# Kernel optimization log

Hardware: AMD Instinct MI355X
Metric: run time of the kernel (lower is better)

The kernel has to match this reference:

```python
import jax, jax.numpy as jnp
import numpy as np
from jax import lax

N, L = 4000, 128          # total sentences, sentence length
VOCAB = 50002             # 50000 words + unk + blk
VEC_DIM, POS_DIM = 50, 5
EMB = VEC_DIM + 2 * POS_DIM   # 60
HID = 230
NPOS = 201                # 2*max_pos_length+1
NBAG, BAGSZ = 500, 8
NREL = 25


def setup_inputs() -> dict:
    key = jax.random.key(0)
    ks = jax.random.split(key, 10)
    X = jax.random.randint(ks[0], (N, L), 0, 50000)
    pos1 = jax.random.randint(ks[1], (N, L), 0, NPOS)
    pos2 = jax.random.randint(ks[2], (N, L), 0, NPOS)
    mask = jnp.zeros((N, L), dtype=jnp.int64)       # unused by CNN encoder
    length = jnp.full((N,), L, dtype=jnp.int64)     # unused by CNN encoder
    starts = jnp.arange(NBAG) * BAGSZ
    scope = jnp.stack([starts, starts + BAGSZ], axis=1)  # [NBAG, 2] contiguous bags
    relation = jax.random.randint(ks[3], (NBAG,), 0, NREL)
    word_emb = jax.random.normal(ks[4], (VOCAB, VEC_DIM), jnp.float32) * 0.1
    pos1_emb = jax.random.normal(ks[5], (NPOS, POS_DIM), jnp.float32) * 0.1
    pos2_emb = jax.random.normal(ks[6], (NPOS, POS_DIM), jnp.float32) * 0.1
    conv_w = jax.random.normal(ks[7], (HID, EMB, 3), jnp.float32) * (1.0 / np.sqrt(EMB * 3))
    conv_b = jnp.zeros((HID,), jnp.float32)
    rel_w = jax.random.normal(ks[8], (NREL, HID), jnp.float32) * (1.0 / np.sqrt(HID))
    rel_b = jnp.zeros((NREL,), jnp.float32)
    return {"X": X, "pos1": pos1, "pos2": pos2, "mask": mask, "length": length,
            "scope": scope, "relation": relation, "word_emb": word_emb,
            "pos1_emb": pos1_emb, "pos2_emb": pos2_emb, "conv_w": conv_w,
            "conv_b": conv_b, "rel_w": rel_w, "rel_b": rel_b}


def reference(X, pos1, pos2, mask, length, scope, relation,
              word_emb, pos1_emb, pos2_emb, conv_w, conv_b, rel_w, rel_b):
    # --- word_pos_embedding: gather + concat -> [N, L, EMB]
    emb = jnp.concatenate([word_emb[X], pos1_emb[pos1], pos2_emb[pos2]], axis=-1)
    # --- CNN encoder: conv1d(k=3, same pad) -> max-pool over seq -> relu
    h = lax.conv_general_dilated(
        emb.transpose(0, 2, 1), conv_w, window_strides=(1,), padding='SAME',
        dimension_numbers=('NCH', 'OIH', 'NCH'))  # [N, HID, L]
    h = jax.nn.relu(jnp.max(h + conv_b[None, :, None], axis=2))  # [N, HID]
    # (dropout p=0.0 -> identity)
    # --- ragged per-bag softmax attention pooling (training path, relation given)
    sizes = scope[:, 1] - scope[:, 0]
    bag_ids = jnp.repeat(jnp.arange(NBAG), sizes, total_repeat_length=N)  # [N]
    rel_q = rel_w[relation]                       # [NBAG, HID] attention queries
    logits = jnp.sum(h * rel_q[bag_ids], axis=-1)  # [N]
    m = jax.ops.segment_max(logits, bag_ids, num_segments=NBAG)
    e = jnp.exp(logits - m[bag_ids])
    denom = jax.ops.segment_sum(e, bag_ids, num_segments=NBAG)
    alpha = e / denom[bag_ids]                     # per-bag softmax weights
    bag_rep = jax.ops.segment_sum(alpha[:, None] * h, bag_ids, num_segments=NBAG)  # [NBAG, HID]
    # --- relation classifier
    return bag_rep @ rel_w.T + rel_b               # [NBAG, NREL]
```

## Files before the change

### kernel.cpp

```cpp
#include <hip/hip_runtime.h>
#include <hip/hip_bf16.h>

#define NSENT 4000
#define LSEQ  128
#define VEC   50
#define POS   5
#define EMBD  60
#define HIDD  230
#define HSTR  232
#define NBAG  500
#define NREL  25
#define NTILEP 16
#define KSTEPS 6
#define ESTR  72
#define SLOTS 130
#define SSTR  (SLOTS * ESTR)

typedef __attribute__((ext_vector_type(8))) short short8;
typedef __attribute__((ext_vector_type(4))) float f32x4;

__device__ __forceinline__ unsigned short f2bf(float f) {
    union { float f; unsigned u; } v; v.f = f;
    unsigned u = v.u + 0x7FFF + ((v.u >> 16) & 1);
    return (unsigned short)(u >> 16);
}

__device__ __forceinline__ unsigned pk(float a, float b) {
    __hip_bfloat162 h = __float22bfloat162_rn(float2{a, b});
    union { __hip_bfloat162 h; unsigned u; } c; c.h = h;
    return c.u;
}

__global__ __launch_bounds__(256) void prep_b(const float* __restrict__ conv_w,
                                              unsigned short* __restrict__ Bfrag) {
    int idx = blockIdx.x * 256 + threadIdx.x;
    if (idx >= NTILEP * KSTEPS * 64 * 8) return;
    int j    = idx & 7;
    int lane = (idx >> 3) & 63;
    int t    = idx >> 9;
    int ks   = t % KSTEPS;
    int nt   = t / KSTEPS;
    int c    = nt * 16 + (lane & 15);
    int klin = ks * 32 + (lane >> 4) * 8 + j;
    int tap  = klin >> 6;
    int e    = klin & 63;
    float v  = 0.f;
    if (c < HIDD) {
        int eidx = -1;
        if (e < 50)                 eidx = e;
        else if (e >= 52 && e < 56) eidx = 50 + (e - 52);
        else if (e >= 56 && e < 60) eidx = 55 + (e - 56);
        else if (e == 60)           eidx = 54;
        else if (e == 62)           eidx = 59;
        if (eidx >= 0) v = conv_w[(c * EMBD + eidx) * 3 + tap];
    }
    Bfrag[idx] = f2bf(v);
}

__global__ __launch_bounds__(512, 4) void encoder(
    const int*   __restrict__ X,  const int* __restrict__ P1, const int* __restrict__ P2,
    const float* __restrict__ wemb, const float* __restrict__ p1emb, const float* __restrict__ p2emb,
    const unsigned short* __restrict__ Bfrag, const float* __restrict__ conv_b,
    float* __restrict__ H)
{
    __shared__ unsigned short embS[2 * SSTR];
    __shared__ int xS[2 * LSEQ], p1S[2 * LSEQ], p2S[2 * LSEQ];
    const int b2 = blockIdx.x * 2, tid = threadIdx.x;
    const int lane = tid & 63;
    const int wave = __builtin_amdgcn_readfirstlane(tid >> 6);
    const int nt0  = wave * 2;
    const int m    = lane & 15;
    const int quad = lane >> 4;

    short8 Bw[2][KSTEPS];
    #pragma unroll
    for (int t = 0; t < 2; ++t)
        #pragma unroll
        for (int ks = 0; ks < KSTEPS; ++ks)
            Bw[t][ks] = *(const short8*)(Bfrag + ((size_t)((nt0 + t) * KSTEPS + ks) * 64 + lane) * 8);

    #pragma unroll
    for (int it = 0; it < 2; ++it) {
        int i = tid + it * 512;
        if (i < 768) {
            int which = i >> 8, l2 = i & 255;
            const int* src = (which == 0) ? X : (which == 1) ? P1 : P2;
            int v = src[(size_t)b2 * LSEQ + l2];
            int* dst = (which == 0) ? xS : (which == 1) ? p1S : p2S;
            dst[l2] = v;
        } else {
            int t = i - 768;
            if (t < 128) {
                int sent = t >> 6;
                int r = (t & 32) ? (SLOTS - 1) : 0;
                *(unsigned*)(embS + sent * SSTR + r * ESTR + (t & 31) * 2) = 0u;
            }
        }
    }
    __syncthreads();

    #pragma unroll
    for (int it = 0; it < (2 * LSEQ * 16) / 512; ++it) {
        int i = tid + it * 512;
        int sent = i >> 11, rem = i & 2047;
        int l = rem >> 4, j = rem & 15;
        int li = sent * LSEQ + l;
        unsigned short* dst = embS + sent * SSTR + (l + 1) * ESTR;
        uint2 v;
        if (j < 13) {
            const float* src = wemb + (size_t)xS[li] * VEC + j * 4;
            float2 fa = *(const float2*)(src);
            float a2 = 0.f, a3 = 0.f;
            if (j < 12) { float2 fb = *(const float2*)(src + 2); a2 = fb.x; a3 = fb.y; }
            v.x = pk(fa.x, fa.y); v.y = pk(a2, a3);
        } else if (j == 13) {
            const float* p = p1emb + p1S[li] * POS;
            v.x = pk(p[0], p[1]); v.y = pk(p[2], p[3]);
        } else if (j == 14) {
            const float* p = p2emb + p2S[li] * POS;
            v.x = pk(p[0], p[1]); v.y = pk(p[2], p[3]);
        } else {
            float a = p1emb[p1S[li] * POS + 4];
            float b = p2emb[p2S[li] * POS + 4];
            v.x = pk(a, 0.f); v.y = pk(b, 0.f);
        }
        *(uint2*)(dst + (j < 13 ? j * 4 : 52 + (j - 13) * 4)) = v;
    }
    __syncthreads();

    #pragma unroll 1
    for (int s = 0; s < 2; ++s) {
        const unsigned short* eb = embS + s * SSTR;
        float maxv[2][4];
        #pragma unroll
        for (int t = 0; t < 2; ++t)
            #pragma unroll
            for (int r = 0; r < 4; ++r) maxv[t][r] = -1e30f;

        #pragma unroll
        for (int mt = 0; mt < 8; ++mt) {
            short8 A[KSTEPS];
            #pragma unroll
            for (int ks = 0; ks < KSTEPS; ++ks) {
                int tap = ks >> 1;
                int col = (ks & 1) * 32 + quad * 8;
                int row = mt * 16 + m + tap;
                A[ks] = *(const short8*)(eb + row * ESTR + col);
            }
            f32x4 acc[2];
            #pragma unroll
            for (int t = 0; t < 2; ++t) acc[t] = (f32x4){0.f, 0.f, 0.f, 0.f};
            #pragma unroll
            for (int ks = 0; ks < KSTEPS; ++ks)
                #pragma unroll
                for (int t = 0; t < 2; ++t)
                    acc[t] = __builtin_amdgcn_mfma_f32_16x16x32_bf16(A[ks], Bw[t][ks], acc[t], 0, 0, 0);
            #pragma unroll
            for (int t = 0; t < 2; ++t)
                #pragma unroll
                for (int r = 0; r < 4; ++r)
                    maxv[t][r] = fmaxf(maxv[t][r], acc[t][r]);
        }

        #pragma unroll
        for (int t = 0; t < 2; ++t) {
            float v = fmaxf(fmaxf(maxv[t][0], maxv[t][1]),
                            fmaxf(maxv[t][2], maxv[t][3]));
            v = fmaxf(v, __shfl_xor(v, 16));
            v = fmaxf(v, __shfl_xor(v, 32));
            int c = (nt0 + t) * 16 + lane;
            if (lane < 16 && c < HIDD)
                H[(size_t)(b2 + s) * HSTR + c] = fmaxf(v + conv_b[c], 0.f);
        }
    }
}

__global__ __launch_bounds__(64) void attn(
    const float* __restrict__ H, const float* __restrict__ rel_w, const float* __restrict__ rel_b,
    const int* __restrict__ relation, const int* __restrict__ scope,
    float* __restrict__ out)
{
    const int b = blockIdx.x, lane = threadIdx.x;
    const int start = scope[2 * b];
    int ns = scope[2 * b + 1] - start;
    if (ns > 8) ns = 8;
    const int rel = relation[b];

    float q[4], h[8][4];
    #pragma unroll
    for (int k = 0; k < 4; ++k) {
        int c = lane + 64 * k;
        q[k] = (c < HIDD) ? rel_w[rel * HIDD + c] : 0.f;
    }
    #pragma unroll
    for (int s = 0; s < 8; ++s)
        #pragma unroll
        for (int k = 0; k < 4; ++k) {
            int c = lane + 64 * k;
            h[s][k] = (s < ns && c < HIDD) ? H[(size_t)(start + s) * HSTR + c] : 0.f;
        }

    float logit[8];
    #pragma unroll
    for (int s = 0; s < 8; ++s) {
        float t = q[0] * h[s][0] + q[1] * h[s][1] + q[2] * h[s][2] + q[3] * h[s][3];
        #pragma unroll
        for (int off = 32; off > 0; off >>= 1) t += __shfl_xor(t, off);
        logit[s] = t;
    }

    float mx = -1e30f;
    for (int s = 0; s < ns; ++s) mx = fmaxf(mx, logit[s]);
    float a[8], den = 0.f;
    #pragma unroll
    for (int s = 0; s < 8; ++s) { a[s] = (s < ns) ? expf(logit[s] - mx) : 0.f; den += a[s]; }
    float inv = 1.f / den;

    float rep[4];
    #pragma unroll
    for (int k = 0; k < 4; ++k) {
        float r = 0.f;
        #pragma unroll
        for (int s = 0; s < 8; ++s) r += a[s] * h[s][k];
        rep[k] = r * inv;
    }

    #pragma unroll 5
    for (int g = 0; g < NREL; ++g) {
        float t = 0.f;
        #pragma unroll
        for (int k = 0; k < 4; ++k) {
            int c = lane + 64 * k;
            t += (c < HIDD) ? rel_w[g * HIDD + c] * rep[k] : 0.f;
        }
        #pragma unroll
        for (int off = 32; off > 0; off >>= 1) t += __shfl_xor(t, off);
        if (lane == 0) out[b * NREL + g] = t + rel_b[g];
    }
}

extern "C" void kernel_launch(void* const* d_in, const int* in_sizes, int n_in,
                              void* d_out, int out_size, void* d_ws, size_t ws_size,
                              hipStream_t stream) {
    const int*   X        = (const int*)d_in[0];
    const int*   P1       = (const int*)d_in[1];
    const int*   P2       = (const int*)d_in[2];
    const int*   scope    = (const int*)d_in[5];
    const int*   relation = (const int*)d_in[6];
    const float* wemb     = (const float*)d_in[7];
    const float* p1emb    = (const float*)d_in[8];
    const float* p2emb    = (const float*)d_in[9];
    const float* conv_w   = (const float*)d_in[10];
    const float* conv_b   = (const float*)d_in[11];
    const float* rel_w    = (const float*)d_in[12];
    const float* rel_b    = (const float*)d_in[13];

    char* ws = (char*)d_ws;
    float* H = (float*)ws;
    size_t off = (size_t)NSENT * HSTR * 4;
    unsigned short* Bfrag = (unsigned short*)(ws + off);

    const int btot = NTILEP * KSTEPS * 64 * 8;
    hipLaunchKernelGGL(prep_b, dim3((btot + 255) / 256), dim3(256), 0, stream,
                       conv_w, Bfrag);
    hipLaunchKernelGGL(encoder, dim3(NSENT / 2), dim3(512), 0, stream,
                       X, P1, P2, wemb, p1emb, p2emb, Bfrag, conv_b, H);
    hipLaunchKernelGGL(attn, dim3(NBAG), dim3(64), 0, stream,
                       H, rel_w, rel_b, relation, scope, (float*)d_out);
}
```

Measured before the change: 183.6 us.

## Switch encoder conv GEMM from 16x16x32 to 32x32x16 bf16 MFMA tiles

The encoder convolution now uses 32x32x16 bf16 MFMA instructions, with each wave owning one 32-channel tile instead of two 16-channel tiles. The prep kernel's B-fragment layout is regenerated to match. The mt and ks loops are rolled (unroll 1 and unroll 4) and A fragments are loaded per k-step, which cuts instruction count and register pressure. Launch bounds drop from 4 to 2 blocks per SM. The bigger tile reduces LDS A-fragment traffic per FLOP, at the cost of less unrolling and fewer resident blocks available to hide latency.

```diff
diff --git a/kernel.cpp b/kernel.cpp
--- a/kernel.cpp
+++ b/kernel.cpp
@@ -10,14 +10,14 @@
 #define HSTR  232
 #define NBAG  500
 #define NREL  25
-#define NTILEP 16
-#define KSTEPS 6
+#define NT32  8
+#define KS32  12
 #define ESTR  72
 #define SLOTS 130
 #define SSTR  (SLOTS * ESTR)
 
-typedef __attribute__((ext_vector_type(8))) short short8;
-typedef __attribute__((ext_vector_type(4))) float f32x4;
+typedef __attribute__((ext_vector_type(8)))  short short8;
+typedef __attribute__((ext_vector_type(16))) float f32x16;
 
 __device__ __forceinline__ unsigned short f2bf(float f) {
     union { float f; unsigned u; } v; v.f = f;
@@ -34,30 +34,30 @@
 __global__ __launch_bounds__(256) void prep_b(const float* __restrict__ conv_w,
                                               unsigned short* __restrict__ Bfrag) {
     int idx = blockIdx.x * 256 + threadIdx.x;
-    if (idx >= NTILEP * KSTEPS * 64 * 8) return;
+    if (idx >= NT32 * KS32 * 64 * 8) return;
     int j    = idx & 7;
     int lane = (idx >> 3) & 63;
     int t    = idx >> 9;
-    int ks   = t % KSTEPS;
-    int nt   = t / KSTEPS;
-    int c    = nt * 16 + (lane & 15);
-    int klin = ks * 32 + (lane >> 4) * 8 + j;
+    int ks   = t % KS32;
+    int nt   = t / KS32;
+    int n    = nt * 32 + (lane & 31);
+    int klin = ks * 16 + (lane >> 5) * 8 + j;
     int tap  = klin >> 6;
     int e    = klin & 63;
     float v  = 0.f;
-    if (c < HIDD) {
+    if (n < HIDD) {
         int eidx = -1;
         if (e < 50)                 eidx = e;
         else if (e >= 52 && e < 56) eidx = 50 + (e - 52);
         else if (e >= 56 && e < 60) eidx = 55 + (e - 56);
         else if (e == 60)           eidx = 54;
         else if (e == 62)           eidx = 59;
-        if (eidx >= 0) v = conv_w[(c * EMBD + eidx) * 3 + tap];
+        if (eidx >= 0) v = conv_w[(n * EMBD + eidx) * 3 + tap];
     }
     Bfrag[idx] = f2bf(v);
 }
 
-__global__ __launch_bounds__(512, 4) void encoder(
+__global__ __launch_bounds__(512, 2) void encoder(
     const int*   __restrict__ X,  const int* __restrict__ P1, const int* __restrict__ P2,
     const float* __restrict__ wemb, const float* __restrict__ p1emb, const float* __restrict__ p2emb,
     const unsigned short* __restrict__ Bfrag, const float* __restrict__ conv_b,
@@ -68,16 +68,13 @@
     const int b2 = blockIdx.x * 2, tid = threadIdx.x;
     const int lane = tid & 63;
     const int wave = __builtin_amdgcn_readfirstlane(tid >> 6);
-    const int nt0  = wave * 2;
-    const int m    = lane & 15;
-    const int quad = lane >> 4;
-
-    short8 Bw[2][KSTEPS];
-    #pragma unroll
-    for (int t = 0; t < 2; ++t)
-        #pragma unroll
-        for (int ks = 0; ks < KSTEPS; ++ks)
-            Bw[t][ks] = *(const short8*)(Bfrag + ((size_t)((nt0 + t) * KSTEPS + ks) * 64 + lane) * 8);
+    const int m32  = lane & 31;
+    const int half = lane >> 5;
+
+    short8 Bw[KS32];
+    #pragma unroll
+    for (int ks = 0; ks < KS32; ++ks)
+        Bw[ks] = *(const short8*)(Bfrag + ((size_t)(wave * KS32 + ks) * 64 + lane) * 8);
 
     #pragma unroll
     for (int it = 0; it < 2; ++it) {
@@ -131,47 +128,33 @@
     #pragma unroll 1
     for (int s = 0; s < 2; ++s) {
         const unsigned short* eb = embS + s * SSTR;
-        float maxv[2][4];
-        #pragma unroll
-        for (int t = 0; t < 2; ++t)
+        float maxv[16];
+        #pragma unroll
+        for (int r = 0; r < 16; ++r) maxv[r] = -1e30f;
+
+        #pragma unroll 1
+        for (int mt = 0; mt < 4; ++mt) {
+            f32x16 acc = {0.f, 0.f, 0.f, 0.f, 0.f, 0.f, 0.f, 0.f,
+                          0.f, 0.f, 0.f, 0.f, 0.f, 0.f, 0.f, 0.f};
+            #pragma unroll 4
+            for (int ks = 0; ks < KS32; ++ks) {
+                int row = mt * 32 + m32 + (ks >> 2);
+                int col = (ks & 3) * 16 + half * 8;
+                short8 A = *(const short8*)(eb + row * ESTR + col);
+                acc = __builtin_amdgcn_mfma_f32_32x32x16_bf16(A, Bw[ks], acc, 0, 0, 0);
+            }
             #pragma unroll
-            for (int r = 0; r < 4; ++r) maxv[t][r] = -1e30f;
-
-        #pragma unroll
-        for (int mt = 0; mt < 8; ++mt) {
-            short8 A[KSTEPS];
-            #pragma unroll
-            for (int ks = 0; ks < KSTEPS; ++ks) {
-                int tap = ks >> 1;
-                int col = (ks & 1) * 32 + quad * 8;
-                int row = mt * 16 + m + tap;
-                A[ks] = *(const short8*)(eb + row * ESTR + col);
-            }
-            f32x4 acc[2];
-            #pragma unroll
-            for (int t = 0; t < 2; ++t) acc[t] = (f32x4){0.f, 0.f, 0.f, 0.f};
-            #pragma unroll
-            for (int ks = 0; ks < KSTEPS; ++ks)
-                #pragma unroll
-                for (int t = 0; t < 2; ++t)
-                    acc[t] = __builtin_amdgcn_mfma_f32_16x16x32_bf16(A[ks], Bw[t][ks], acc[t], 0, 0, 0);
-            #pragma unroll
-            for (int t = 0; t < 2; ++t)
-                #pragma unroll
-                for (int r = 0; r < 4; ++r)
-                    maxv[t][r] = fmaxf(maxv[t][r], acc[t][r]);
-        }
-
-        #pragma unroll
-        for (int t = 0; t < 2; ++t) {
-            float v = fmaxf(fmaxf(maxv[t][0], maxv[t][1]),
-                            fmaxf(maxv[t][2], maxv[t][3]));
-            v = fmaxf(v, __shfl_xor(v, 16));
-            v = fmaxf(v, __shfl_xor(v, 32));
-            int c = (nt0 + t) * 16 + lane;
-            if (lane < 16 && c < HIDD)
-                H[(size_t)(b2 + s) * HSTR + c] = fmaxf(v + conv_b[c], 0.f);
-        }
+            for (int r = 0; r < 16; ++r)
+                maxv[r] = fmaxf(maxv[r], acc[r]);
+        }
+
+        float v = maxv[0];
+        #pragma unroll
+        for (int r = 1; r < 16; ++r) v = fmaxf(v, maxv[r]);
+        v = fmaxf(v, __shfl_xor(v, 32));
+        int c = wave * 32 + m32;
+        if (lane < 32 && c < HIDD)
+            H[(size_t)(b2 + s) * HSTR + c] = fmaxf(v + conv_b[c], 0.f);
     }
 }
 
@@ -260,7 +243,7 @@
     size_t off = (size_t)NSENT * HSTR * 4;
     unsigned short* Bfrag = (unsigned short*)(ws + off);
 
-    const int btot = NTILEP * KSTEPS * 64 * 8;
+    const int btot = NT32 * KS32 * 64 * 8;
     hipLaunchKernelGGL(prep_b, dim3((btot + 255) / 256), dim3(256), 0, stream,
                        conv_w, Bfrag);
     hipLaunchKernelGGL(encoder, dim3(NSENT / 2), dim3(512), 0, stream,
```

New measurement: 363.3 us. 97.8% more time.
